# Optimization experiments

Hardware: AMD Instinct MI355X
Metric: run time of the kernel (lower is better)

The kernel has to match this reference:

```python
import jax, jax.numpy as jnp
import numpy as np

B, T, N = 32, 512, 16
C, V, D, H, L = 150, 832, 512, 512, 5  # chord vocab, note vocab, embed dim, hidden, layers


def setup_inputs() -> dict:
    key = jax.random.key(0)
    ks = jax.random.split(key, 16)
    s = 0.05
    note = jax.random.randint(ks[0], (B, T, N), 0, V)
    chord = jax.random.randint(ks[1], (B, T), 0, C)
    chord_table = jax.random.normal(ks[2], (C, D), jnp.float32) * s
    note_table = jax.random.normal(ks[3], (V, D), jnp.float32) * s
    # GRU layer 0 (input = 2*D), layers 1..L-1 (input = H), gate order r,z,n like torch
    w_ih0 = jax.random.normal(ks[4], (3 * H, 2 * D), jnp.float32) * s
    w_hh0 = jax.random.normal(ks[5], (3 * H, H), jnp.float32) * s
    b_ih0 = jax.random.normal(ks[6], (3 * H,), jnp.float32) * s
    b_hh0 = jax.random.normal(ks[7], (3 * H,), jnp.float32) * s
    w_ih_r = jax.random.normal(ks[8], (L - 1, 3 * H, H), jnp.float32) * s
    w_hh_r = jax.random.normal(ks[9], (L - 1, 3 * H, H), jnp.float32) * s
    b_ih_r = jax.random.normal(ks[10], (L - 1, 3 * H), jnp.float32) * s
    b_hh_r = jax.random.normal(ks[11], (L - 1, 3 * H), jnp.float32) * s
    fc_w = jax.random.normal(ks[12], (C, H), jnp.float32) * s
    fc_b = jax.random.normal(ks[13], (C,), jnp.float32) * s
    return dict(note=note, chord=chord, chord_table=chord_table, note_table=note_table,
                w_ih0=w_ih0, w_hh0=w_hh0, b_ih0=b_ih0, b_hh0=b_hh0,
                w_ih_r=w_ih_r, w_hh_r=w_hh_r, b_ih_r=b_ih_r, b_hh_r=b_hh_r,
                fc_w=fc_w, fc_b=fc_b)


def _gru_layer(x, wih, whh, bih, bhh):
    # x: [B, T, in] -> [B, T, H], torch GRU cell math (gate order r,z,n)
    xp = jnp.einsum('bti,gi->btg', x, wih) + bih          # precompute input proj [B,T,3H]
    xp = jnp.swapaxes(xp, 0, 1)                            # [T,B,3H]
    h0 = jnp.zeros((x.shape[0], whh.shape[1]), x.dtype)

    def step(h, xpt):
        gh = h @ whh.T + bhh
        xr, xz, xn = jnp.split(xpt, 3, axis=-1)
        hr, hz, hn = jnp.split(gh, 3, axis=-1)
        r = jax.nn.sigmoid(xr + hr)
        z = jax.nn.sigmoid(xz + hz)
        n = jnp.tanh(xn + r * hn)
        h_new = (1.0 - z) * n + z * h
        return h_new, h_new

    _, ys = jax.lax.scan(step, h0, xp)
    return jnp.swapaxes(ys, 0, 1)                          # [B,T,H]


def _forward(note, chord, chord_table, note_table, w_ih0, w_hh0, b_ih0, b_hh0,
             w_ih_r, w_hh_r, b_ih_r, b_hh_r, fc_w, fc_b):
    # padding_idx=0: zero row 0 of both tables (also blocks its gradient)
    ct = chord_table.at[0].set(0.0)
    nt = note_table.at[0].set(0.0)
    chord_emb = ct[chord]                                   # [B,T,D]
    # ragged mean over notes before first zero; mask[k]=1 iff no zero in note[...,:k+1]
    mask = jnp.cumprod((note != 0).astype(chord_table.dtype), axis=-1)  # [B,T,N]
    emb = nt[note]                                          # [B,T,N,D]
    cnt = jnp.maximum(mask.sum(-1), 1.0)                    # zero_index==0 case -> mean of zero row
    note_emb = jnp.einsum('btnd,btn->btd', emb, mask) / cnt[..., None]
    x = jnp.concatenate([chord_emb, note_emb], axis=-1)     # [B,T,2D]
    x = _gru_layer(x, w_ih0, w_hh0, b_ih0, b_hh0)
    for l in range(w_ih_r.shape[0]):
        x = _gru_layer(x, w_ih_r[l], w_hh_r[l], b_ih_r[l], b_hh_r[l])
    return x @ fc_w.T + fc_b                                # [B,T,C]


def reference(note, chord, chord_table, note_table, w_ih0, w_hh0, b_ih0, b_hh0,
              w_ih_r, w_hh_r, b_ih_r, b_hh_r, fc_w, fc_b):
    return _forward(note, chord, chord_table, note_table, w_ih0, w_hh0, b_ih0, b_hh0,
                    w_ih_r, w_hh_r, b_ih_r, b_hh_r, fc_w, fc_b)
```

## Files before the change

### kernel.cpp

```cpp
#include <hip/hip_runtime.h>
#include <hip/hip_bf16.h>

#define B_   32
#define T_   512
#define NN_  16
#define CV_  150
#define D_   512
#define H_   512
#define BT_  16384
#define K0_  1024
#define G3H_ 1536
#define SUBS_ 32
#define NBF_ 160
#define WSZ_ 49152

using bf16x8 = __attribute__((ext_vector_type(8))) short;
using f32x4  = __attribute__((ext_vector_type(4))) float;
using u32x4  = __attribute__((ext_vector_type(4))) unsigned int;
typedef unsigned long long u64;

__device__ __forceinline__ unsigned short f2bf(float f){
  unsigned int u = __builtin_bit_cast(unsigned int, f);
  u += 0x7fffu + ((u >> 16) & 1u);
  return (unsigned short)(u >> 16);
}

__device__ __forceinline__ void store8(unsigned short* p, f32x4 a, f32x4 b){
  union { unsigned short us[8]; u32x4 v; } u;
  u.us[0]=f2bf(a[0]); u.us[1]=f2bf(a[1]); u.us[2]=f2bf(a[2]); u.us[3]=f2bf(a[3]);
  u.us[4]=f2bf(b[0]); u.us[5]=f2bf(b[1]); u.us[6]=f2bf(b[2]); u.us[7]=f2bf(b[3]);
  *(u32x4*)p = u.v;
}

__device__ __forceinline__ u64 ld_coh_u64(const u64* p){
  return __hip_atomic_load(p, __ATOMIC_RELAXED, __HIP_MEMORY_SCOPE_AGENT);
}
__device__ __forceinline__ void st_coh_u32(void* p, unsigned int v){
  __hip_atomic_store((unsigned int*)p, v, __ATOMIC_RELAXED, __HIP_MEMORY_SCOPE_AGENT);
}
__device__ __forceinline__ void st_flag(int* p, int v){
  __hip_atomic_store(p, v, __ATOMIC_RELAXED, __HIP_MEMORY_SCOPE_AGENT);
}
__device__ __forceinline__ int ld_flag(const int* p){
  return __hip_atomic_load(p, __ATOMIC_RELAXED, __HIP_MEMORY_SCOPE_AGENT);
}

__global__ void convert_bf16(const float* __restrict__ src,
                             unsigned short* __restrict__ dst, int n){
  int i = blockIdx.x * 256 + threadIdx.x;
  if (i < n) dst[i] = f2bf(src[i]);
}

__global__ void prep_wfrag(const float* __restrict__ whh0,
                           const float* __restrict__ whhr,
                           const float* __restrict__ wihr,
                           unsigned short* __restrict__ wsw, int total){
  int idx = blockIdx.x * 256 + threadIdx.x;
  if (idx >= total) return;
  int pos = idx & 511;
  int lam = pos >> 3, e = pos & 7;
  int fr  = idx >> 9;
  int ks  = fr & 31;
  int g   = (fr >> 5) % 3;
  int blk = fr / 96;
  int sub = blk & 31, l = blk >> 5;
  int row = g * 512 + sub * 16 + (lam & 15);
  int k   = (ks & 15) * 32 + (lam >> 4) * 8 + e;
  float v;
  if (l == 0) v = (ks < 16) ? whh0[(size_t)row * H_ + k] : 0.f;
  else {
    const float* w = (ks < 16) ? (whhr + (size_t)(l - 1) * G3H_ * H_)
                               : (wihr + (size_t)(l - 1) * G3H_ * H_);
    v = w[(size_t)row * H_ + k];
  }
  wsw[idx] = f2bf(v);
}

__global__ void prep_bias(const float* __restrict__ bhh0,
                          const float* __restrict__ bihr,
                          const float* __restrict__ bhhr,
                          float* __restrict__ bias_sw, int total){
  int idx = blockIdx.x * 256 + threadIdx.x;
  if (idx >= total) return;
  int q = idx & 3, u = (idx >> 2) & 15, sub = (idx >> 6) & 31, l = idx >> 11;
  int j = sub * 16 + u;
  float v;
  if (l == 0){
    v = (q == 0) ? bhh0[j] : (q == 1) ? bhh0[512 + j] : (q == 2) ? 0.f : bhh0[1024 + j];
  } else {
    const float* bi = bihr + (size_t)(l - 1) * G3H_;
    const float* bh = bhhr + (size_t)(l - 1) * G3H_;
    v = (q == 0) ? bi[j] + bh[j]
      : (q == 1) ? bi[512 + j] + bh[512 + j]
      : (q == 2) ? bi[1024 + j] : bh[1024 + j];
  }
  bias_sw[idx] = v;
}

__global__ __launch_bounds__(64) void emb_kernel(
    const int* __restrict__ note, const int* __restrict__ chord,
    const float* __restrict__ ctab, const float* __restrict__ ntab,
    unsigned short* __restrict__ x0){
  const int bt = blockIdx.x;
  const int tid = threadIdx.x;
  __shared__ int sn[NN_];
  if (tid < NN_) sn[tid] = note[bt * NN_ + tid];
  __syncthreads();
  float alive = 1.f, cnt = 0.f;
  float msk[NN_];
  #pragma unroll
  for (int k = 0; k < NN_; ++k){ if (sn[k] == 0) alive = 0.f; msk[k] = alive; cnt += alive; }
  const float inv = 1.f / fmaxf(cnt, 1.f);
  const int ch = chord[bt];
  const int d0 = tid * 8;
  f32x4 c0 = {0.f,0.f,0.f,0.f}, c1 = {0.f,0.f,0.f,0.f};
  if (ch != 0){
    const float* cp = ctab + (size_t)ch * D_ + d0;
    c0 = *(const f32x4*)cp; c1 = *(const f32x4*)(cp + 4);
  }
  f32x4 s0 = {0.f,0.f,0.f,0.f}, s1 = {0.f,0.f,0.f,0.f};
  #pragma unroll
  for (int k = 0; k < NN_; ++k){
    if (msk[k] != 0.f){
      const float* np = ntab + (size_t)sn[k] * D_ + d0;
      s0 += *(const f32x4*)np;
      s1 += *(const f32x4*)(np + 4);
    }
  }
  s0 *= inv; s1 *= inv;
  unsigned short* o = x0 + (size_t)bt * K0_ + d0;
  store8(o, c0, c1);
  store8(o + D_, s0, s1);
}

__global__ __launch_bounds__(256) void gemm_bt(
    const unsigned short* __restrict__ X, const unsigned short* __restrict__ W,
    const float* __restrict__ bias, float* __restrict__ Y,
    int M, int N, int K, int wmode){
  const int lane = threadIdx.x & 63;
  const int wave = threadIdx.x >> 6;
  const int l15 = lane & 15, kq4 = lane >> 4;
  const int m_frag = blockIdx.y * 64 + wave * 16 + l15;
  const int n_base = blockIdx.x * 64;
  f32x4 acc[4] = {{0.f,0.f,0.f,0.f},{0.f,0.f,0.f,0.f},{0.f,0.f,0.f,0.f},{0.f,0.f,0.f,0.f}};
  const unsigned short* xptr = X + (size_t)m_frag * K + kq4 * 8;
  const unsigned short* wptr[4];
  #pragma unroll
  for (int i = 0; i < 4; ++i){
    int n = n_base + i * 16 + l15;
    if (n >= N) n = N - 1;
    wptr[i] = W + (size_t)n * K + kq4 * 8;
  }
  for (int k0 = 0; k0 < K; k0 += 32){
    bf16x8 a = *(const bf16x8*)(xptr + k0);
    #pragma unroll
    for (int i = 0; i < 4; ++i){
      bf16x8 b = *(const bf16x8*)(wptr[i] + k0);
      acc[i] = __builtin_amdgcn_mfma_f32_16x16x32_bf16(a, b, acc[i], 0, 0, 0);
    }
  }
  const int mrow = blockIdx.y * 64 + wave * 16 + kq4 * 4;
  #pragma unroll
  for (int i = 0; i < 4; ++i){
    int n = n_base + i * 16 + l15;
    if (n < N){
      float bv = bias[n];
      #pragma unroll
      for (int r = 0; r < 4; ++r){
        int m = mrow + r;
        float v = acc[i][r] + bv;
        if (wmode == 0) Y[(size_t)m * N + n] = v;
        else            Y[((size_t)(m & (T_-1)) * N + n) * B_ + (m >> 9)] = v;
      }
    }
  }
}

__global__ __launch_bounds__(256, 1) void gru_fused(
    const float* __restrict__ xp, const unsigned short* __restrict__ wsw,
    const float* __restrict__ bias_sw, unsigned short* __restrict__ hT,
    unsigned short* __restrict__ xT, unsigned short* __restrict__ xout,
    int* __restrict__ flags){
  __shared__ unsigned short w_s[96 * 512];
  __shared__ unsigned short stage_s[32 * 512];
  __shared__ float p_s[4][2][16][16];

  const int tid = threadIdx.x;
  const int blk = blockIdx.x;
  const int l   = blk >> 5;
  const int sub = blk & 31;
  const int lane = tid & 63, wave = tid >> 6;
  const int l15 = lane & 15, l4 = lane >> 4;
  const int myn = wave >> 1;
  const bool rzw = (wave & 1) == 0;

  {
    const u32x4* src = (const u32x4*)(wsw + (size_t)blk * WSZ_);
    u32x4* dst = (u32x4*)w_s;
    #pragma unroll
    for (int i = 0; i < 24; ++i) dst[tid + 256 * i] = src[tid + 256 * i];
  }

  const int cb = tid & 31;
  const int cj = (tid >> 5) * 2;
  const int jg = sub * 16 + cj;
  const float* bsp = bias_sw + blk * 64;
  const float br0 = bsp[cj*4+0],     bz0 = bsp[cj*4+1],     bx0 = bsp[cj*4+2],     bn0 = bsp[cj*4+3];
  const float br1 = bsp[(cj+1)*4+0], bz1 = bsp[(cj+1)*4+1], bx1 = bsp[(cj+1)*4+2], bn1 = bsp[(cj+1)*4+3];
  float hres0 = 0.f, hres1 = 0.f;

  unsigned short* hTl = hT + (size_t)l * (2 * 32 * 512);
  unsigned short* xTw = xT + (size_t)l * (4 * 32 * 512);
  const unsigned short* xTr = xT + (size_t)(l - 1) * (4 * 32 * 512);
  int*       fl_own  = flags + l * 64;
  const int* fl_prod = flags + (l > 0 ? (l - 1) * 64 : l * 64);
  const int* fl_cons = flags + (l + 1) * 64;

  __syncthreads();

  for (int t = 0; t < T_; ++t){
    if (wave == 0){
      const int* pp; int tgt;
      if (lane < 32){ pp = fl_own + lane; tgt = t; }
      else if (l > 0){ pp = fl_prod + (lane - 32); tgt = t + 1; }
      else { pp = fl_own + (lane - 32); tgt = -(1 << 30); }
      while (true){ int v = ld_flag(pp); if (__all(v >= tgt)) break; }
    } else if (wave == 1 && l < 4){
      const int* pp = fl_cons + (lane & 31);
      const int tgt = t - 3;
      while (true){
        int v = (lane < 32) ? ld_flag(pp) : 0x7fffffff;
        if (__all(v >= tgt)) break;
      }
    }
    __syncthreads();

    float er = 0.f, ez = 0.f, en = 0.f, er1 = 0.f, ez1 = 0.f, en1 = 0.f;
    if (l == 0){
      const float* xb = xp + (size_t)t * (G3H_ * B_) + cb;
      er  = xb[(size_t)(0 * H_ + jg) * B_];  er1 = xb[(size_t)(0 * H_ + jg + 1) * B_];
      ez  = xb[(size_t)(1 * H_ + jg) * B_];  ez1 = xb[(size_t)(1 * H_ + jg + 1) * B_];
      en  = xb[(size_t)(2 * H_ + jg) * B_];  en1 = xb[(size_t)(2 * H_ + jg + 1) * B_];
    }

    {
      const unsigned short* hsrc = hTl + (size_t)(t & 1) * (32 * 512);
      u64 lo[8], hi[8];
      #pragma unroll
      for (int i = 0; i < 8; ++i){
        int c = tid + 256 * i;
        int f = c >> 6, lam = c & 63;
        int b = ((f >> 4) << 4) | (lam & 15);
        int k = ((f & 15) << 5) | ((lam >> 4) << 3);
        const u64* sp = (const u64*)(hsrc + b * 512 + k);
        lo[i] = ld_coh_u64(sp);
        hi[i] = ld_coh_u64(sp + 1);
      }
      #pragma unroll
      for (int i = 0; i < 8; ++i){
        int c = tid + 256 * i;
        *(u64*)&stage_s[c * 8]     = lo[i];
        *(u64*)&stage_s[c * 8 + 4] = hi[i];
      }
    }

    union Ufrag { u64 q[2]; bf16x8 v; };
    Ufrag xb[16];
    if (l > 0){
      const unsigned short* xs = xTr + (size_t)(t & 3) * (32 * 512)
                               + (size_t)(myn * 16 + l15) * 512 + l4 * 8;
      #pragma unroll
      for (int ks = 0; ks < 16; ++ks){
        const u64* sp = (const u64*)(xs + ks * 32);
        xb[ks].q[0] = ld_coh_u64(sp);
        xb[ks].q[1] = ld_coh_u64(sp + 1);
      }
    }
    __syncthreads();

    f32x4 accA = {0.f,0.f,0.f,0.f}, accB = {0.f,0.f,0.f,0.f};
    #pragma unroll
    for (int ks = 0; ks < 16; ++ks){
      bf16x8 b = *(const bf16x8*)&stage_s[((myn << 4) + ks) * 512 + lane * 8];
      if (rzw){
        bf16x8 a0 = *(const bf16x8*)&w_s[(0 * 32 + ks) * 512 + lane * 8];
        bf16x8 a1 = *(const bf16x8*)&w_s[(1 * 32 + ks) * 512 + lane * 8];
        accA = __builtin_amdgcn_mfma_f32_16x16x32_bf16(a0, b, accA, 0, 0, 0);
        accB = __builtin_amdgcn_mfma_f32_16x16x32_bf16(a1, b, accB, 0, 0, 0);
      } else {
        bf16x8 a2 = *(const bf16x8*)&w_s[(2 * 32 + ks) * 512 + lane * 8];
        accA = __builtin_amdgcn_mfma_f32_16x16x32_bf16(a2, b, accA, 0, 0, 0);
      }
    }
    if (l > 0){
      #pragma unroll
      for (int ks = 0; ks < 16; ++ks){
        bf16x8 b = xb[ks].v;
        if (rzw){
          bf16x8 a0 = *(const bf16x8*)&w_s[(0 * 32 + 16 + ks) * 512 + lane * 8];
          bf16x8 a1 = *(const bf16x8*)&w_s[(1 * 32 + 16 + ks) * 512 + lane * 8];
          accA = __builtin_amdgcn_mfma_f32_16x16x32_bf16(a0, b, accA, 0, 0, 0);
          accB = __builtin_amdgcn_mfma_f32_16x16x32_bf16(a1, b, accB, 0, 0, 0);
        } else {
          bf16x8 a2 = *(const bf16x8*)&w_s[(2 * 32 + 16 + ks) * 512 + lane * 8];
          accB = __builtin_amdgcn_mfma_f32_16x16x32_bf16(a2, b, accB, 0, 0, 0);
        }
      }
    }
    #pragma unroll
    for (int r = 0; r < 4; ++r){
      int u = l4 * 4 + r;
      if (rzw){ p_s[0][myn][u][l15] = accA[r]; p_s[1][myn][u][l15] = accB[r]; }
      else    { p_s[2][myn][u][l15] = accA[r]; p_s[3][myn][u][l15] = accB[r]; }
    }
    __syncthreads();

    {
      const int nt = cb >> 4, bc = cb & 15;
      float rp0 = p_s[0][nt][cj][bc],     rp1 = p_s[0][nt][cj + 1][bc];
      float zp0 = p_s[1][nt][cj][bc],     zp1 = p_s[1][nt][cj + 1][bc];
      float hp0 = p_s[2][nt][cj][bc],     hp1 = p_s[2][nt][cj + 1][bc];
      float xq0 = p_s[3][nt][cj][bc],     xq1 = p_s[3][nt][cj + 1][bc];
      float r0 = 1.f / (1.f + __expf(-(rp0 + er  + br0)));
      float r1 = 1.f / (1.f + __expf(-(rp1 + er1 + br1)));
      float z0 = 1.f / (1.f + __expf(-(zp0 + ez  + bz0)));
      float z1 = 1.f / (1.f + __expf(-(zp1 + ez1 + bz1)));
      float nx0 = (l > 0) ? (xq0 + bx0) : en;
      float nx1 = (l > 0) ? (xq1 + bx1) : en1;
      float e0 = __expf(2.f * (nx0 + r0 * (hp0 + bn0)));
      float e1 = __expf(2.f * (nx1 + r1 * (hp1 + bn1)));
      float n0 = (e0 - 1.f) / (e0 + 1.f);
      float n1 = (e1 - 1.f) / (e1 + 1.f);
      float h0 = (1.f - z0) * n0 + z0 * hres0; hres0 = h0;
      float h1 = (1.f - z1) * n1 + z1 * hres1; hres1 = h1;
      unsigned int pk = (unsigned int)f2bf(h0) | ((unsigned int)f2bf(h1) << 16);
      st_coh_u32(hTl + (size_t)((t + 1) & 1) * (32 * 512) + cb * 512 + jg, pk);
      if (l < 4) st_coh_u32(xTw + (size_t)(t & 3) * (32 * 512) + cb * 512 + jg, pk);
      else *(unsigned int*)&xout[((size_t)cb * T_ + t) * H_ + jg] = pk;
    }
    __syncthreads();
    if (tid == 0) st_flag(fl_own + sub, t + 1);
  }
}

extern "C" void kernel_launch(void* const* d_in, const int* in_sizes, int n_in,
                              void* d_out, int out_size, void* d_ws, size_t ws_size,
                              hipStream_t stream){
  (void)in_sizes; (void)n_in; (void)out_size; (void)ws_size;
  const int*   note  = (const int*)d_in[0];
  const int*   chord = (const int*)d_in[1];
  const float* ctab  = (const float*)d_in[2];
  const float* ntab  = (const float*)d_in[3];
  const float* wih0  = (const float*)d_in[4];
  const float* whh0  = (const float*)d_in[5];
  const float* bih0  = (const float*)d_in[6];
  const float* bhh0  = (const float*)d_in[7];
  const float* wihr  = (const float*)d_in[8];
  const float* whhr  = (const float*)d_in[9];
  const float* bihr  = (const float*)d_in[10];
  const float* bhhr  = (const float*)d_in[11];
  const float* fcw   = (const float*)d_in[12];
  const float* fcb   = (const float*)d_in[13];
  float* out = (float*)d_out;

  char* ws = (char*)d_ws;
  size_t off = 0;
  auto alloc = [&](size_t bytes)->char*{
    char* p = ws + off; off = (off + bytes + 255) & ~(size_t)255; return p;
  };
  int*            flags   = (int*)alloc((size_t)5 * 64 * sizeof(int));
  float*          xp      = (float*)alloc((size_t)BT_ * G3H_ * 4);
  unsigned short* x0      = (unsigned short*)alloc((size_t)BT_ * K0_ * 2);
  unsigned short* xout    = (unsigned short*)alloc((size_t)BT_ * H_ * 2);
  unsigned short* hT      = (unsigned short*)alloc((size_t)5 * 2 * 32 * 512 * 2);
  unsigned short* xT      = (unsigned short*)alloc((size_t)4 * 4 * 32 * 512 * 2);
  unsigned short* wsw     = (unsigned short*)alloc((size_t)NBF_ * WSZ_ * 2);
  float*          bias_sw = (float*)alloc((size_t)NBF_ * 64 * 4);
  unsigned short* wih0_b  = (unsigned short*)alloc((size_t)G3H_ * K0_ * 2);
  unsigned short* fcw_b   = (unsigned short*)alloc((size_t)CV_ * H_ * 2);

  hipMemsetAsync(flags, 0, (size_t)5 * 64 * sizeof(int), stream);
  hipMemsetAsync(hT, 0, (size_t)5 * 2 * 32 * 512 * 2, stream);

  { int n = G3H_ * K0_; convert_bf16<<<(n + 255) / 256, 256, 0, stream>>>(wih0, wih0_b, n); }
  { int n = CV_ * H_;   convert_bf16<<<(n + 255) / 256, 256, 0, stream>>>(fcw, fcw_b, n); }
  { int n = NBF_ * WSZ_;
    prep_wfrag<<<(n + 255) / 256, 256, 0, stream>>>(whh0, whhr, wihr, wsw, n); }
  { int n = NBF_ * 64;
    prep_bias<<<(n + 255) / 256, 256, 0, stream>>>(bhh0, bihr, bhhr, bias_sw, n); }

  emb_kernel<<<BT_, 64, 0, stream>>>(note, chord, ctab, ntab, x0);

  gemm_bt<<<dim3(G3H_ / 64, BT_ / 64), 256, 0, stream>>>(x0, wih0_b, bih0, xp, BT_, G3H_, K0_, 1);

  gru_fused<<<NBF_, 256, 0, stream>>>(xp, wsw, bias_sw, hT, xT, xout, flags);

  gemm_bt<<<dim3((CV_ + 63) / 64, BT_ / 64), 256, 0, stream>>>(
      xout, fcw_b, fcb, out, BT_, CV_, H_, 0);
}
```

Before: 6.035 ms.

## Replace per-step flag barriers with sentinel-poisoned ring buffers in fused GRU

Removes the per-timestep flag polling and the two block barriers on flag waits. Consumers now spin directly on the hidden and input ring-buffer data until no sentinel values remain, and producers poison slots ahead of time. Deeper rings (8 hidden slots, 32 input slots) need backpressure only every fourth step. The wave split also changes: each wave computes all three gates over half of K, the partial sums are reduced through a double-buffered shared array, and layer-0 input projections are prefetched two steps ahead. The trade-offs are sentinel collision risk (a bf16 pair equal to 0x7f7f), iteration caps that could let stale data through, extra memsets, and workspace overlap between x0/wih0 and the ring buffers.

```diff
diff --git a/kernel.cpp b/kernel.cpp
--- a/kernel.cpp
+++ b/kernel.cpp
@@ -10,9 +10,15 @@
 #define BT_  16384
 #define K0_  1024
 #define G3H_ 1536
-#define SUBS_ 32
 #define NBF_ 160
 #define WSZ_ 49152
+#define XSLOT_ 16384
+#define XRING_ 32
+#define HRING_ 8
+#define SENT32 0x7f7f7f7fu
+#define HCAP 4096
+#define XCAP 4096
+#define BCAP 65536
 
 using bf16x8 = __attribute__((ext_vector_type(8))) short;
 using f32x4  = __attribute__((ext_vector_type(4))) float;
@@ -43,6 +49,10 @@
 }
 __device__ __forceinline__ int ld_flag(const int* p){
   return __hip_atomic_load(p, __ATOMIC_RELAXED, __HIP_MEMORY_SCOPE_AGENT);
+}
+
+__device__ __forceinline__ bool bad64(u64 q){
+  return ((unsigned int)q == SENT32) | ((unsigned int)(q >> 32) == SENT32);
 }
 
 __global__ void convert_bf16(const float* __restrict__ src,
@@ -176,23 +186,19 @@
   }
 }
 
+union Ufrag { u64 q[2]; bf16x8 v; };
+
 __global__ __launch_bounds__(256, 1) void gru_fused(
     const float* __restrict__ xp, const unsigned short* __restrict__ wsw,
-    const float* __restrict__ bias_sw, unsigned short* __restrict__ hT,
-    unsigned short* __restrict__ xT, unsigned short* __restrict__ xout,
-    int* __restrict__ flags){
+    const float* __restrict__ bias_sw, unsigned short* hT,
+    unsigned short* xT, unsigned short* xout, int* cprog){
   __shared__ unsigned short w_s[96 * 512];
-  __shared__ unsigned short stage_s[32 * 512];
-  __shared__ float p_s[4][2][16][16];
+  __shared__ float p_s[2][4][2][2][16][16];
 
   const int tid = threadIdx.x;
   const int blk = blockIdx.x;
   const int l   = blk >> 5;
   const int sub = blk & 31;
-  const int lane = tid & 63, wave = tid >> 6;
-  const int l15 = lane & 15, l4 = lane >> 4;
-  const int myn = wave >> 1;
-  const bool rzw = (wave & 1) == 0;
 
   {
     const u32x4* src = (const u32x4*)(wsw + (size_t)blk * WSZ_);
@@ -200,6 +206,16 @@
     #pragma unroll
     for (int i = 0; i < 24; ++i) dst[tid + 256 * i] = src[tid + 256 * i];
   }
+  __syncthreads();
+
+  const int lane = tid & 63, wave = tid >> 6;
+  const int l15 = lane & 15, l4 = lane >> 4;
+  const int myn = wave >> 1;
+  const int kh  = wave & 1;
+  const int myb = (myn << 4) + l15;
+  const int fro = (l4 << 3);
+  const int khofs = kh * 256;
+  const int khb = kh * 8;
 
   const int cb = tid & 31;
   const int cj = (tid >> 5) * 2;
@@ -209,124 +225,149 @@
   const float br1 = bsp[(cj+1)*4+0], bz1 = bsp[(cj+1)*4+1], bx1 = bsp[(cj+1)*4+2], bn1 = bsp[(cj+1)*4+3];
   float hres0 = 0.f, hres1 = 0.f;
 
-  unsigned short* hTl = hT + (size_t)l * (2 * 32 * 512);
-  unsigned short* xTw = xT + (size_t)l * (4 * 32 * 512);
-  const unsigned short* xTr = xT + (size_t)(l - 1) * (4 * 32 * 512);
-  int*       fl_own  = flags + l * 64;
-  const int* fl_prod = flags + (l > 0 ? (l - 1) * 64 : l * 64);
-  const int* fl_cons = flags + (l + 1) * 64;
-
-  __syncthreads();
+  unsigned short* hTl = hT + (size_t)l * (HRING_ * 32 * 512);
+  unsigned short* xTw = xT + (size_t)(l < 4 ? l : 0) * ((size_t)XRING_ * XSLOT_);
+  const unsigned short* xTr = xT + (size_t)(l > 0 ? l - 1 : 0) * ((size_t)XRING_ * XSLOT_);
+  const int* bp_own = cprog + (l << 5);
+  int*       bp_pub = cprog + ((l > 0 ? l - 1 : 0) << 5);
+
+  float era=0,eza=0,ena=0,era1=0,eza1=0,ena1=0;
+  float erb=0,ezb=0,enb=0,erb1=0,ezb1=0,enb1=0;
+  if (l == 0){
+    { const float* xq = xp + (size_t)0 * (G3H_ * B_) + cb;
+      era=xq[(size_t)(0*H_+jg)*B_]; era1=xq[(size_t)(0*H_+jg+1)*B_];
+      eza=xq[(size_t)(1*H_+jg)*B_]; eza1=xq[(size_t)(1*H_+jg+1)*B_];
+      ena=xq[(size_t)(2*H_+jg)*B_]; ena1=xq[(size_t)(2*H_+jg+1)*B_]; }
+    { const float* xq = xp + (size_t)1 * (G3H_ * B_) + cb;
+      erb=xq[(size_t)(0*H_+jg)*B_]; erb1=xq[(size_t)(0*H_+jg+1)*B_];
+      ezb=xq[(size_t)(1*H_+jg)*B_]; ezb1=xq[(size_t)(1*H_+jg+1)*B_];
+      enb=xq[(size_t)(2*H_+jg)*B_]; enb1=xq[(size_t)(2*H_+jg+1)*B_]; }
+  }
 
   for (int t = 0; t < T_; ++t){
-    if (wave == 0){
-      const int* pp; int tgt;
-      if (lane < 32){ pp = fl_own + lane; tgt = t; }
-      else if (l > 0){ pp = fl_prod + (lane - 32); tgt = t + 1; }
-      else { pp = fl_own + (lane - 32); tgt = -(1 << 30); }
-      while (true){ int v = ld_flag(pp); if (__all(v >= tgt)) break; }
-    } else if (wave == 1 && l < 4){
-      const int* pp = fl_cons + (lane & 31);
-      const int tgt = t - 3;
+    const int pb = t & 1;
+
+    Ufrag hb[8];
+    const unsigned short* hf = hTl + (((size_t)(t & HRING_-1) * 32 + myb) << 9) + khofs + fro;
+    #pragma unroll
+    for (int j = 0; j < 8; ++j){
+      const u64* sp = (const u64*)(hf + (j << 5));
+      hb[j].q[0] = ld_coh_u64(sp); hb[j].q[1] = ld_coh_u64(sp + 1);
+    }
+    {
+      int itc = 0;
       while (true){
-        int v = (lane < 32) ? ld_flag(pp) : 0x7fffffff;
-        if (__all(v >= tgt)) break;
-      }
-    }
-    __syncthreads();
-
-    float er = 0.f, ez = 0.f, en = 0.f, er1 = 0.f, ez1 = 0.f, en1 = 0.f;
+        int nbad = 0;
+        #pragma unroll
+        for (int j = 0; j < 8; ++j){
+          bool bd = bad64(hb[j].q[0]) | bad64(hb[j].q[1]);
+          if (__any((int)bd)){
+            ++nbad;
+            const u64* sp = (const u64*)(hf + (j << 5));
+            hb[j].q[0] = ld_coh_u64(sp); hb[j].q[1] = ld_coh_u64(sp + 1);
+          }
+        }
+        if (nbad == 0) break;
+        if (++itc > HCAP) break;
+      }
+    }
+
+    Ufrag xb[8];
+    const unsigned short* xs = nullptr;
+    if (l > 0){
+      xs = xTr + (size_t)(t & XRING_-1) * XSLOT_ + (size_t)myb * 512 + khofs + fro;
+      #pragma unroll
+      for (int j = 0; j < 8; ++j){
+        const u64* sp = (const u64*)(xs + (j << 5));
+        xb[j].q[0] = ld_coh_u64(sp); xb[j].q[1] = ld_coh_u64(sp + 1);
+      }
+    }
+
+    if (l < 4 && t && (t & 3) == 0){
+      int itc = 0;
+      while (true){
+        int v = (lane < 32) ? ld_flag(&bp_own[lane]) : 0x7fffffff;
+        if (__all(v >= t - 4)) break;
+        if (++itc > BCAP) break;
+        __builtin_amdgcn_s_sleep(2);
+      }
+    }
+
+    f32x4 accR = {0.f,0.f,0.f,0.f}, accZ = {0.f,0.f,0.f,0.f};
+    f32x4 accN = {0.f,0.f,0.f,0.f}, accX = {0.f,0.f,0.f,0.f};
+    #pragma unroll
+    for (int j = 0; j < 8; ++j){
+      bf16x8 b  = hb[j].v;
+      bf16x8 a0 = *(const bf16x8*)&w_s[(0 * 32 + khb + j) * 512 + lane * 8];
+      bf16x8 a1 = *(const bf16x8*)&w_s[(1 * 32 + khb + j) * 512 + lane * 8];
+      bf16x8 a2 = *(const bf16x8*)&w_s[(2 * 32 + khb + j) * 512 + lane * 8];
+      accR = __builtin_amdgcn_mfma_f32_16x16x32_bf16(a0, b, accR, 0, 0, 0);
+      accZ = __builtin_amdgcn_mfma_f32_16x16x32_bf16(a1, b, accZ, 0, 0, 0);
+      accN = __builtin_amdgcn_mfma_f32_16x16x32_bf16(a2, b, accN, 0, 0, 0);
+    }
+
+    if (l > 0){
+      int itc = 0;
+      while (true){
+        int nbad = 0;
+        #pragma unroll
+        for (int j = 0; j < 8; ++j){
+          bool bd = bad64(xb[j].q[0]) | bad64(xb[j].q[1]);
+          if (__any((int)bd)){
+            ++nbad;
+            const u64* sp = (const u64*)(xs + (j << 5));
+            xb[j].q[0] = ld_coh_u64(sp); xb[j].q[1] = ld_coh_u64(sp + 1);
+          }
+        }
+        if (nbad == 0) break;
+        if (++itc > XCAP) break;
+      }
+      #pragma unroll
+      for (int j = 0; j < 8; ++j){
+        bf16x8 b  = xb[j].v;
+        bf16x8 a0 = *(const bf16x8*)&w_s[(0 * 32 + 16 + khb + j) * 512 + lane * 8];
+        bf16x8 a1 = *(const bf16x8*)&w_s[(1 * 32 + 16 + khb + j) * 512 + lane * 8];
+        bf16x8 a2 = *(const bf16x8*)&w_s[(2 * 32 + 16 + khb + j) * 512 + lane * 8];
+        accR = __builtin_amdgcn_mfma_f32_16x16x32_bf16(a0, b, accR, 0, 0, 0);
+        accZ = __builtin_amdgcn_mfma_f32_16x16x32_bf16(a1, b, accZ, 0, 0, 0);
+        accX = __builtin_amdgcn_mfma_f32_16x16x32_bf16(a2, b, accX, 0, 0, 0);
+      }
+    }
+
+    float erc=0,ezc=0,enc=0,erc1=0,ezc1=0,enc1=0;
     if (l == 0){
-      const float* xb = xp + (size_t)t * (G3H_ * B_) + cb;
-      er  = xb[(size_t)(0 * H_ + jg) * B_];  er1 = xb[(size_t)(0 * H_ + jg + 1) * B_];
-      ez  = xb[(size_t)(1 * H_ + jg) * B_];  ez1 = xb[(size_t)(1 * H_ + jg + 1) * B_];
-      en  = xb[(size_t)(2 * H_ + jg) * B_];  en1 = xb[(size_t)(2 * H_ + jg + 1) * B_];
-    }
-
-    {
-      const unsigned short* hsrc = hTl + (size_t)(t & 1) * (32 * 512);
-      u64 lo[8], hi[8];
-      #pragma unroll
-      for (int i = 0; i < 8; ++i){
-        int c = tid + 256 * i;
-        int f = c >> 6, lam = c & 63;
-        int b = ((f >> 4) << 4) | (lam & 15);
-        int k = ((f & 15) << 5) | ((lam >> 4) << 3);
-        const u64* sp = (const u64*)(hsrc + b * 512 + k);
-        lo[i] = ld_coh_u64(sp);
-        hi[i] = ld_coh_u64(sp + 1);
-      }
-      #pragma unroll
-      for (int i = 0; i < 8; ++i){
-        int c = tid + 256 * i;
-        *(u64*)&stage_s[c * 8]     = lo[i];
-        *(u64*)&stage_s[c * 8 + 4] = hi[i];
-      }
-    }
-
-    union Ufrag { u64 q[2]; bf16x8 v; };
-    Ufrag xb[16];
-    if (l > 0){
-      const unsigned short* xs = xTr + (size_t)(t & 3) * (32 * 512)
-                               + (size_t)(myn * 16 + l15) * 512 + l4 * 8;
-      #pragma unroll
-      for (int ks = 0; ks < 16; ++ks){
-        const u64* sp = (const u64*)(xs + ks * 32);
-        xb[ks].q[0] = ld_coh_u64(sp);
-        xb[ks].q[1] = ld_coh_u64(sp + 1);
-      }
-    }
-    __syncthreads();
-
-    f32x4 accA = {0.f,0.f,0.f,0.f}, accB = {0.f,0.f,0.f,0.f};
-    #pragma unroll
-    for (int ks = 0; ks < 16; ++ks){
-      bf16x8 b = *(const bf16x8*)&stage_s[((myn << 4) + ks) * 512 + lane * 8];
-      if (rzw){
-        bf16x8 a0 = *(const bf16x8*)&w_s[(0 * 32 + ks) * 512 + lane * 8];
-        bf16x8 a1 = *(const bf16x8*)&w_s[(1 * 32 + ks) * 512 + lane * 8];
-        accA = __builtin_amdgcn_mfma_f32_16x16x32_bf16(a0, b, accA, 0, 0, 0);
-        accB = __builtin_amdgcn_mfma_f32_16x16x32_bf16(a1, b, accB, 0, 0, 0);
-      } else {
-        bf16x8 a2 = *(const bf16x8*)&w_s[(2 * 32 + ks) * 512 + lane * 8];
-        accA = __builtin_amdgcn_mfma_f32_16x16x32_bf16(a2, b, accA, 0, 0, 0);
-      }
-    }
-    if (l > 0){
-      #pragma unroll
-      for (int ks = 0; ks < 16; ++ks){
-        bf16x8 b = xb[ks].v;
-        if (rzw){
-          bf16x8 a0 = *(const bf16x8*)&w_s[(0 * 32 + 16 + ks) * 512 + lane * 8];
-          bf16x8 a1 = *(const bf16x8*)&w_s[(1 * 32 + 16 + ks) * 512 + lane * 8];
-          accA = __builtin_amdgcn_mfma_f32_16x16x32_bf16(a0, b, accA, 0, 0, 0);
-          accB = __builtin_amdgcn_mfma_f32_16x16x32_bf16(a1, b, accB, 0, 0, 0);
-        } else {
-          bf16x8 a2 = *(const bf16x8*)&w_s[(2 * 32 + 16 + ks) * 512 + lane * 8];
-          accB = __builtin_amdgcn_mfma_f32_16x16x32_bf16(a2, b, accB, 0, 0, 0);
-        }
-      }
-    }
+      const float* xq = xp + (size_t)((t + 2) & (T_ - 1)) * (G3H_ * B_) + cb;
+      erc=xq[(size_t)(0*H_+jg)*B_]; erc1=xq[(size_t)(0*H_+jg+1)*B_];
+      ezc=xq[(size_t)(1*H_+jg)*B_]; ezc1=xq[(size_t)(1*H_+jg+1)*B_];
+      enc=xq[(size_t)(2*H_+jg)*B_]; enc1=xq[(size_t)(2*H_+jg+1)*B_];
+    }
+
     #pragma unroll
     for (int r = 0; r < 4; ++r){
       int u = l4 * 4 + r;
-      if (rzw){ p_s[0][myn][u][l15] = accA[r]; p_s[1][myn][u][l15] = accB[r]; }
-      else    { p_s[2][myn][u][l15] = accA[r]; p_s[3][myn][u][l15] = accB[r]; }
+      p_s[pb][0][myn][kh][u][l15] = accR[r];
+      p_s[pb][1][myn][kh][u][l15] = accZ[r];
+      p_s[pb][2][myn][kh][u][l15] = accN[r];
+      p_s[pb][3][myn][kh][u][l15] = accX[r];
     }
     __syncthreads();
 
     {
       const int nt = cb >> 4, bc = cb & 15;
-      float rp0 = p_s[0][nt][cj][bc],     rp1 = p_s[0][nt][cj + 1][bc];
-      float zp0 = p_s[1][nt][cj][bc],     zp1 = p_s[1][nt][cj + 1][bc];
-      float hp0 = p_s[2][nt][cj][bc],     hp1 = p_s[2][nt][cj + 1][bc];
-      float xq0 = p_s[3][nt][cj][bc],     xq1 = p_s[3][nt][cj + 1][bc];
-      float r0 = 1.f / (1.f + __expf(-(rp0 + er  + br0)));
-      float r1 = 1.f / (1.f + __expf(-(rp1 + er1 + br1)));
-      float z0 = 1.f / (1.f + __expf(-(zp0 + ez  + bz0)));
-      float z1 = 1.f / (1.f + __expf(-(zp1 + ez1 + bz1)));
-      float nx0 = (l > 0) ? (xq0 + bx0) : en;
-      float nx1 = (l > 0) ? (xq1 + bx1) : en1;
+      float rp0 = p_s[pb][0][nt][0][cj][bc]   + p_s[pb][0][nt][1][cj][bc];
+      float rp1 = p_s[pb][0][nt][0][cj+1][bc] + p_s[pb][0][nt][1][cj+1][bc];
+      float zp0 = p_s[pb][1][nt][0][cj][bc]   + p_s[pb][1][nt][1][cj][bc];
+      float zp1 = p_s[pb][1][nt][0][cj+1][bc] + p_s[pb][1][nt][1][cj+1][bc];
+      float hp0 = p_s[pb][2][nt][0][cj][bc]   + p_s[pb][2][nt][1][cj][bc];
+      float hp1 = p_s[pb][2][nt][0][cj+1][bc] + p_s[pb][2][nt][1][cj+1][bc];
+      float xq0 = p_s[pb][3][nt][0][cj][bc]   + p_s[pb][3][nt][1][cj][bc];
+      float xq1 = p_s[pb][3][nt][0][cj+1][bc] + p_s[pb][3][nt][1][cj+1][bc];
+      float r0 = 1.f / (1.f + __expf(-(rp0 + era  + br0)));
+      float r1 = 1.f / (1.f + __expf(-(rp1 + era1 + br1)));
+      float z0 = 1.f / (1.f + __expf(-(zp0 + eza  + bz0)));
+      float z1 = 1.f / (1.f + __expf(-(zp1 + eza1 + bz1)));
+      float nx0 = (l > 0) ? (xq0 + bx0) : ena;
+      float nx1 = (l > 0) ? (xq1 + bx1) : ena1;
       float e0 = __expf(2.f * (nx0 + r0 * (hp0 + bn0)));
       float e1 = __expf(2.f * (nx1 + r1 * (hp1 + bn1)));
       float n0 = (e0 - 1.f) / (e0 + 1.f);
@@ -334,12 +375,22 @@
       float h0 = (1.f - z0) * n0 + z0 * hres0; hres0 = h0;
       float h1 = (1.f - z1) * n1 + z1 * hres1; hres1 = h1;
       unsigned int pk = (unsigned int)f2bf(h0) | ((unsigned int)f2bf(h1) << 16);
-      st_coh_u32(hTl + (size_t)((t + 1) & 1) * (32 * 512) + cb * 512 + jg, pk);
-      if (l < 4) st_coh_u32(xTw + (size_t)(t & 3) * (32 * 512) + cb * 512 + jg, pk);
-      else *(unsigned int*)&xout[((size_t)cb * T_ + t) * H_ + jg] = pk;
-    }
-    __syncthreads();
-    if (tid == 0) st_flag(fl_own + sub, t + 1);
+
+      st_coh_u32(hTl + (((size_t)((t + 1) & HRING_-1) * 32 + cb) << 9) + jg, pk);
+      st_coh_u32(hTl + (((size_t)((t + 4) & HRING_-1) * 32 + cb) << 9) + jg, SENT32);
+
+      if (l < 4){
+        st_coh_u32(xTw + (size_t)(t & XRING_-1) * XSLOT_ + (size_t)cb * 512 + jg, pk);
+        st_coh_u32(xTw + (size_t)((t + 16) & XRING_-1) * XSLOT_ + (size_t)cb * 512 + jg, SENT32);
+      } else {
+        *(unsigned int*)&xout[((size_t)cb * T_ + t) * H_ + jg] = pk;
+      }
+
+      if (l > 0 && (t & 3) == 3 && tid == 0) st_flag(&bp_pub[sub], t);
+
+      era = erb; eza = ezb; ena = enb; era1 = erb1; eza1 = ezb1; ena1 = enb1;
+      erb = erc; ezb = ezc; enb = enc; erb1 = erc1; ezb1 = ezc1; enb1 = enc1;
+    }
   }
 }
 
@@ -368,19 +419,26 @@
   auto alloc = [&](size_t bytes)->char*{
     char* p = ws + off; off = (off + bytes + 255) & ~(size_t)255; return p;
   };
-  int*            flags   = (int*)alloc((size_t)5 * 64 * sizeof(int));
+  int*            cprog   = (int*)alloc(160 * sizeof(int));
   float*          xp      = (float*)alloc((size_t)BT_ * G3H_ * 4);
-  unsigned short* x0      = (unsigned short*)alloc((size_t)BT_ * K0_ * 2);
-  unsigned short* xout    = (unsigned short*)alloc((size_t)BT_ * H_ * 2);
-  unsigned short* hT      = (unsigned short*)alloc((size_t)5 * 2 * 32 * 512 * 2);
-  unsigned short* xT      = (unsigned short*)alloc((size_t)4 * 4 * 32 * 512 * 2);
   unsigned short* wsw     = (unsigned short*)alloc((size_t)NBF_ * WSZ_ * 2);
   float*          bias_sw = (float*)alloc((size_t)NBF_ * 64 * 4);
-  unsigned short* wih0_b  = (unsigned short*)alloc((size_t)G3H_ * K0_ * 2);
   unsigned short* fcw_b   = (unsigned short*)alloc((size_t)CV_ * H_ * 2);
-
-  hipMemsetAsync(flags, 0, (size_t)5 * 64 * sizeof(int), stream);
-  hipMemsetAsync(hT, 0, (size_t)5 * 2 * 32 * 512 * 2, stream);
+  unsigned short* xout    = (unsigned short*)alloc((size_t)BT_ * H_ * 2);
+  const size_t hT_bytes = (size_t)5 * HRING_ * 32 * 512 * 2;
+  const size_t hT_al    = (hT_bytes + 255) & ~(size_t)255;
+  const size_t xT_bytes = (size_t)4 * XRING_ * XSLOT_ * 2;
+  const size_t p2_bytes = hT_al + xT_bytes;
+  const size_t x0_bytes = (size_t)BT_ * K0_ * 2;
+  const size_t x0_al    = (x0_bytes + 255) & ~(size_t)255;
+  const size_t p1_bytes = x0_al + (size_t)G3H_ * K0_ * 2;
+  char* ovl = alloc(p1_bytes > p2_bytes ? p1_bytes : p2_bytes);
+  unsigned short* x0     = (unsigned short*)ovl;
+  unsigned short* wih0_b = (unsigned short*)(ovl + x0_al);
+  unsigned short* hT     = (unsigned short*)ovl;
+  unsigned short* xT     = (unsigned short*)(ovl + hT_al);
+
+  hipMemsetAsync(cprog, 0, 160 * sizeof(int), stream);
 
   { int n = G3H_ * K0_; convert_bf16<<<(n + 255) / 256, 256, 0, stream>>>(wih0, wih0_b, n); }
   { int n = CV_ * H_;   convert_bf16<<<(n + 255) / 256, 256, 0, stream>>>(fcw, fcw_b, n); }
@@ -391,9 +449,15 @@
 
   emb_kernel<<<BT_, 64, 0, stream>>>(note, chord, ctab, ntab, x0);
 
-  gemm_bt<<<dim3(G3H_ / 64, BT_ / 64), 256, 0, stream>>>(x0, wih0_b, bih0, xp, BT_, G3H_, K0_, 1);
-
-  gru_fused<<<NBF_, 256, 0, stream>>>(xp, wsw, bias_sw, hT, xT, xout, flags);
+  gemm_bt<<<dim3(G3H_ / 64, BT_ / 64), 256, 0, stream>>>(
+      x0, wih0_b, bih0, xp, BT_, G3H_, K0_, 1);
+
+  hipMemsetAsync(hT, 0x7F, hT_bytes, stream);
+  for (int ll = 0; ll < 5; ++ll)
+    hipMemsetAsync(hT + (size_t)ll * (HRING_ * 32 * 512), 0, 32 * 512 * 2, stream);
+  hipMemsetAsync(xT, 0x7F, xT_bytes, stream);
+
+  gru_fused<<<NBF_, 256, 0, stream>>>(xp, wsw, bias_sw, hT, xT, xout, cprog);
 
   gemm_bt<<<dim3((CV_ + 63) / 64, BT_ / 64), 256, 0, stream>>>(
       xout, fcw_b, fcb, out, BT_, CV_, H_, 0);
```

After: 6.433 ms. +6.6%, slower.
